# Performance work log

Hardware: AMD Instinct MI355X
Metric: run time of the kernel (lower is better)

## Reference

```python
import jax, jax.numpy as jnp
import numpy as np

B, S, NH, HD = 2, 4096, 16, 64


def setup_inputs() -> dict:
    key = jax.random.key(0)
    kq, kk, kv = jax.random.split(key, 3)
    q = jax.random.normal(kq, (B, S, NH, HD), dtype=jnp.float32)
    k = jax.random.normal(kk, (B, S, NH, HD), dtype=jnp.float32)
    v = jax.random.normal(kv, (B, S, NH, HD), dtype=jnp.float32)
    return {"q": q, "k": k, "v": v}


def reference(q, k, v):
    # SDPA.__call__ with attention_mask=None, segment_ids=None, is_causal=True, dropout=identity
    q_len, nheads, kv_len = q.shape[-3], q.shape[-2], k.shape[-3]
    qs = q / jnp.sqrt(jnp.asarray(q.shape[-1], q.dtype))
    scores = jnp.einsum('...tnh,...snh->...tns', qs, k)  # [B, q, nheads, kv]
    # causal mask: tril over (q, kv), broadcast over heads axis (-2)
    causal = jnp.tril(jnp.ones((q_len, kv_len), dtype=jnp.bool_))[:, None, :]
    neg_inf = jnp.finfo(scores.dtype).min
    scores = jnp.where(causal, scores, neg_inf)
    weights = jax.nn.softmax(scores.astype(jnp.float32), axis=-1).astype(scores.dtype)
    attn = jnp.einsum('...tns,...snh->...tnh', weights, v)
    return attn
```

## Files before the change

kernel.cpp:

```cpp
#include <hip/hip_runtime.h>


constexpr int BATCH  = 2;
constexpr int SEQ    = 4096;
constexpr int NHEADS = 16;
constexpr int HDIM   = 64;
constexpr int ROWSTR = NHEADS * HDIM;
constexpr int BM     = 128;
constexpr int BN     = 64;
constexpr int QTILES = SEQ / BM;
constexpr int BH     = BATCH * NHEADS;

typedef __attribute__((ext_vector_type(8)))  short v8s;
typedef __attribute__((ext_vector_type(16))) float v16f;
typedef __attribute__((ext_vector_type(4)))  unsigned int v4u;
typedef __attribute__((ext_vector_type(2)))  unsigned int v2u;
typedef __attribute__((ext_vector_type(2)))  __bf16 v2bf;

__device__ __forceinline__ unsigned pkbf(float a, float b) {
#if __has_builtin(__builtin_amdgcn_cvt_pk_bf16_f32)
    return __builtin_bit_cast(unsigned, __builtin_amdgcn_cvt_pk_bf16_f32(a, b));
#else
    unsigned ua = __float_as_uint(a); ua += 0x7FFFu + ((ua >> 16) & 1u);
    unsigned ub = __float_as_uint(b); ub += 0x7FFFu + ((ub >> 16) & 1u);
    return (ua >> 16) | (ub & 0xFFFF0000u);
#endif
}

__device__ __forceinline__ int fswz(int r) { return (r & 7) ^ ((r >> 3) & 3); }

__device__ __forceinline__ void async16(const unsigned short* g, unsigned short* l) {
    __builtin_amdgcn_global_load_lds(
        (const __attribute__((address_space(1))) unsigned int*)g,
        (__attribute__((address_space(3))) unsigned int*)l, 16, 0, 0);
}

__global__ __launch_bounds__(256, 4)
void prep(const float* __restrict__ kf, const float* __restrict__ vf,
          unsigned short* __restrict__ kb, unsigned short* __restrict__ vt)
{
    __shared__ unsigned int lds[128 * 33];
    const int tid = threadIdx.x;
    const int blk = (int)blockIdx.x;

    if (blk < 1024) {
        const float4* src = (const float4*)kf + (size_t)blk * 2048;
        unsigned int* dst = (unsigned int*)kb + (size_t)blk * 4096;
        #pragma unroll
        for (int i = 0; i < 8; ++i) {
            const int n = i * 256 + tid;
            float4 f = src[n];
            *(v2u*)(dst + (size_t)n * 2) = (v2u){pkbf(f.x, f.y), pkbf(f.z, f.w)};
        }
        return;
    }

    const int t  = blk - 1024;
    const int b  = t >> 9;
    const int h  = (t >> 5) & 15;
    const int s0 = (t & 31) * 128;

    {
        const float4* vff = (const float4*)vf + (size_t)b * SEQ * 256;
        const int c2 = (tid & 15) * 2;
        #pragma unroll
        for (int i = 0; i < 8; ++i) {
            const int srow = i * 16 + (tid >> 4);
            float4 f = vff[(size_t)(s0 + srow) * 256 + h * 16 + (tid & 15)];
            lds[srow * 33 + c2]     = pkbf(f.x, f.y);
            lds[srow * 33 + c2 + 1] = pkbf(f.z, f.w);
        }
    }
    __syncthreads();
    {
        const int w    = tid >> 6;
        const int lane = tid & 63;
        const int sh   = (lane & 1) * 16;
        const unsigned int* lcol = &lds[w * 32 * 33 + (lane >> 1)];
        unsigned int out[16];
        #pragma unroll
        for (int j = 0; j < 16; ++j) {
            const unsigned a = lcol[(2 * j)     * 33];
            const unsigned c = lcol[(2 * j + 1) * 33];
            out[j] = ((a >> sh) & 0xFFFFu) | (((c >> sh) & 0xFFFFu) << 16);
        }
        unsigned int* dst = (unsigned int*)vt
            + ((size_t)((b * NHEADS + h) * HDIM + lane)) * (SEQ / 2)
            + ((s0 + w * 32) >> 1);
        #pragma unroll
        for (int j = 0; j < 4; ++j)
            *(v4u*)(dst + 4 * j) = (v4u){out[4*j], out[4*j+1], out[4*j+2], out[4*j+3]};
    }
}

__global__ __launch_bounds__(256, 4)
void fa_fwd(const float* __restrict__ qf, const unsigned short* __restrict__ kb,
            const unsigned short* __restrict__ vt, float* __restrict__ og)
{
    __shared__ __align__(16) unsigned short k_s[2][64 * 64];
    __shared__ __align__(16) unsigned short v_s[2][64 * 64];

    const int tid  = threadIdx.x;
    const int wave = tid >> 6;
    const int lane = tid & 63;
    const int hh   = lane >> 5;
    const int l32  = lane & 31;

    const int n  = (int)blockIdx.x;
    const int qtile = QTILES - 1 - (n >> 5);
    const int bh = n & 31;
    const int b = bh >> 4, h = bh & 15;
    const int qbase = qtile * BM;
    const int jmax  = 2 * qtile + 2;

    const int lrow  = lane >> 3;
    const int lcol8 = (lane & 7) ^ lrow ^ wave;
    const int fx = (l32 & 7) ^ ((l32 >> 3) & 3);

    {
        const int krow = tid >> 2;
        const int kc   = (tid & 3) * 16;
        const int sg0  = (2 * (tid & 3))     ^ fswz(krow);
        const int sg1  = (2 * (tid & 3) + 1) ^ fswz(krow);
        const float sc = 0.125f * 1.44269504088896340736f;
        #pragma unroll
        for (int half = 0; half < 2; ++half) {
            const float4* src = (const float4*)(qf +
                ((size_t)((b * SEQ + qbase + half * 64 + krow) * NHEADS + h)) * HDIM + kc);
            float4 f0 = src[0], f1 = src[1], f2 = src[2], f3 = src[3];
            unsigned short* dst = half ? &v_s[0][krow * 64] : &k_s[0][krow * 64];
            *(v4u*)&dst[sg0 * 8] = (v4u){pkbf(f0.x*sc, f0.y*sc), pkbf(f0.z*sc, f0.w*sc),
                                         pkbf(f1.x*sc, f1.y*sc), pkbf(f1.z*sc, f1.w*sc)};
            *(v4u*)&dst[sg1 * 8] = (v4u){pkbf(f2.x*sc, f2.y*sc), pkbf(f2.z*sc, f2.w*sc),
                                         pkbf(f3.x*sc, f3.y*sc), pkbf(f3.z*sc, f3.w*sc)};
        }
    }
    __syncthreads();
    v8s bq[4];
    {
        const int R = wave * 32 + l32;
        const unsigned short* qrow = (R < 64) ? &k_s[0][R * 64] : &v_s[0][(R - 64) * 64];
        #pragma unroll
        for (int c = 0; c < 4; ++c)
            bq[c] = *(const v8s*)&qrow[(((2*c + hh) ^ fswz(R & 63)) * 8)];
    }
    __syncthreads();

    const unsigned short* kgb = kb + (size_t)b * SEQ * ROWSTR + (size_t)h * HDIM;
    const unsigned short* vgb = vt + (size_t)bh * HDIM * SEQ;

    #pragma unroll
    for (int i = 0; i < 2; ++i) {
        const int rbase = i * 32 + wave * 8;
        async16(kgb + (size_t)(rbase + lrow) * ROWSTR + lcol8 * 8, &k_s[0][rbase * 64]);
        async16(vgb + (size_t)(rbase + lrow) * SEQ    + lcol8 * 8, &v_s[0][rbase * 64]);
    }

    const v16f vzero = (v16f)(0.f);
    v16f o_acc[2];
    o_acc[0] = (v16f)(0.f); o_acc[1] = (v16f)(0.f);
    float l_lane = 0.f;
    const int q_abs = qbase + wave * 32 + l32;

#if __has_builtin(__builtin_amdgcn_fdot2_f32_bf16)
    const v2bf ones2 = __builtin_bit_cast(v2bf, 0x3F803F80u);
#endif

    for (int jt = 0; jt < jmax; ++jt) {
        const int buf = jt & 1;
        __syncthreads();

        if (jt + 1 < jmax) {
            const int nb  = (jt + 1) & 1;
            const int kb2 = (jt + 1) * BN;
            #pragma unroll
            for (int i = 0; i < 2; ++i) {
                const int rbase = i * 32 + wave * 8;
                async16(kgb + (size_t)(kb2 + rbase + lrow) * ROWSTR + lcol8 * 8, &k_s[nb][rbase * 64]);
                async16(vgb + (size_t)(rbase + lrow) * SEQ + kb2    + lcol8 * 8, &v_s[nb][rbase * 64]);
            }
        }

        v16f sacc[2];
        __builtin_amdgcn_s_setprio(1);
        #pragma unroll
        for (int mt = 0; mt < 2; ++mt) {
            const int r = mt * 32 + l32;
            {
                v8s ak = *(const v8s*)&k_s[buf][r * 64 + ((hh ^ fx) * 8)];
                sacc[mt] = __builtin_amdgcn_mfma_f32_32x32x16_bf16(ak, bq[0], vzero, 0, 0, 0);
            }
            #pragma unroll
            for (int c = 1; c < 4; ++c) {
                v8s ak = *(const v8s*)&k_s[buf][r * 64 + (((2*c + hh) ^ fx) * 8)];
                sacc[mt] = __builtin_amdgcn_mfma_f32_32x32x16_bf16(ak, bq[c], sacc[mt], 0, 0, 0);
            }
        }
        __builtin_amdgcn_s_setprio(0);

        const bool masked = (jt >= jmax - 2);
        v8s pf4[4];

        auto exppack = [&](v16f& sc, v8s& d0, v8s& d1, int kofs) {
            #pragma unroll
            for (int r = 0; r < 16; ++r) {
                float pv = __builtin_amdgcn_exp2f(sc[r]);
                if (masked) {
                    const int k_abs = kofs + (r & 3) + 8 * (r >> 2) + 4 * hh;
                    pv = (k_abs > q_abs) ? 0.f : pv;
                }
                sc[r] = pv;
#if !__has_builtin(__builtin_amdgcn_fdot2_f32_bf16)
                l_lane += pv;
#endif
            }
            #pragma unroll
            for (int cc = 0; cc < 2; ++cc) {
                const unsigned lo0 = pkbf(sc[8*cc+0], sc[8*cc+1]);
                const unsigned lo1 = pkbf(sc[8*cc+2], sc[8*cc+3]);
                const unsigned hi0 = pkbf(sc[8*cc+4], sc[8*cc+5]);
                const unsigned hi1 = pkbf(sc[8*cc+6], sc[8*cc+7]);
#if __has_builtin(__builtin_amdgcn_fdot2_f32_bf16)
                l_lane = __builtin_amdgcn_fdot2_f32_bf16(__builtin_bit_cast(v2bf, lo0), ones2, l_lane, false);
                l_lane = __builtin_amdgcn_fdot2_f32_bf16(__builtin_bit_cast(v2bf, lo1), ones2, l_lane, false);
                l_lane = __builtin_amdgcn_fdot2_f32_bf16(__builtin_bit_cast(v2bf, hi0), ones2, l_lane, false);
                l_lane = __builtin_amdgcn_fdot2_f32_bf16(__builtin_bit_cast(v2bf, hi1), ones2, l_lane, false);
#endif
#if __has_builtin(__builtin_amdgcn_permlane32_swap)
                auto r0 = __builtin_amdgcn_permlane32_swap(lo0, hi0, false, false);
                auto r1 = __builtin_amdgcn_permlane32_swap(lo1, hi1, false, false);
                (cc ? d1 : d0) = __builtin_bit_cast(v8s, (v4u){r0[0], r1[0], r0[1], r1[1]});
#else
                const unsigned s0 = hh ? lo0 : hi0;
                const unsigned s1 = hh ? lo1 : hi1;
                const unsigned t0 = (unsigned)__shfl_xor((int)s0, 32, 64);
                const unsigned t1 = (unsigned)__shfl_xor((int)s1, 32, 64);
                v4u w;
                w.x = hh ? t0 : lo0;
                w.y = hh ? t1 : lo1;
                w.z = hh ? hi0 : t0;
                w.w = hh ? hi1 : t1;
                (cc ? d1 : d0) = __builtin_bit_cast(v8s, w);
#endif
            }
        };

        exppack(sacc[0], pf4[0], pf4[1], jt * 64);

        __builtin_amdgcn_s_setprio(1);
        #pragma unroll
        for (int nt = 0; nt < 2; ++nt) {
            const int r = nt * 32 + l32;
            #pragma unroll
            for (int c = 0; c < 2; ++c) {
                v8s bv = *(const v8s*)&v_s[buf][r * 64 + (((2*c + hh) ^ fx) * 8)];
                o_acc[nt] = __builtin_amdgcn_mfma_f32_32x32x16_bf16(pf4[c], bv, o_acc[nt], 0, 0, 0);
            }
        }
        __builtin_amdgcn_s_setprio(0);

        exppack(sacc[1], pf4[2], pf4[3], jt * 64 + 32);

        __builtin_amdgcn_s_setprio(1);
        #pragma unroll
        for (int nt = 0; nt < 2; ++nt) {
            const int r = nt * 32 + l32;
            #pragma unroll
            for (int c = 2; c < 4; ++c) {
                v8s bv = *(const v8s*)&v_s[buf][r * 64 + (((2*c + hh) ^ fx) * 8)];
                o_acc[nt] = __builtin_amdgcn_mfma_f32_32x32x16_bf16(pf4[c], bv, o_acc[nt], 0, 0, 0);
            }
        }
        __builtin_amdgcn_s_setprio(0);
    }

    const float lt = l_lane + __shfl_xor(l_lane, 32);

    #pragma unroll
    for (int r = 0; r < 16; ++r) {
        const int q_local = (r & 3) + 8 * (r >> 2) + 4 * hh;
        const float inv_l = 1.0f / __shfl(lt, q_local, 32);
        const int qrow = qbase + wave * 32 + q_local;
        float* dst = og + ((size_t)((b * SEQ + qrow) * NHEADS + h)) * HDIM + l32;
        dst[0]  = o_acc[0][r] * inv_l;
        dst[32] = o_acc[1][r] * inv_l;
    }
}

extern "C" void kernel_launch(void* const* d_in, const int* in_sizes, int n_in,
                              void* d_out, int out_size, void* d_ws, size_t ws_size,
                              hipStream_t stream) {
    const float* q = (const float*)d_in[0];
    const float* k = (const float*)d_in[1];
    const float* v = (const float*)d_in[2];
    float* out = (float*)d_out;

    const size_t TEN = (size_t)BATCH * NHEADS * SEQ * HDIM;
    unsigned short* kbuf = (unsigned short*)d_ws;
    unsigned short* vbuf = kbuf + TEN;

    prep<<<2048, 256, 0, stream>>>(k, v, kbuf, vbuf);
    fa_fwd<<<QTILES * BH, 256, 0, stream>>>(q, kbuf, vbuf, out);
}
```

Measured before the change: 240.9 us.

## Split long causal query tiles across two blocks and combine partial outputs

For the 16 longest causal query tiles, the KV loop is split into two chunks handled by separate blocks. Each chunk writes its unnormalized output and row sums to workspace, and a new combine kernel adds the pairs and normalizes them. The goal is to cut the critical path set by the longest-running blocks in the causally imbalanced grid. The cost is an extra kernel launch plus workspace traffic for the partials. A fallback path that reorders tile scheduling is used when the workspace is too small.

```diff
diff --git a/kernel.cpp b/kernel.cpp
--- a/kernel.cpp
+++ b/kernel.cpp
@@ -10,6 +10,7 @@
 constexpr int BN     = 64;
 constexpr int QTILES = SEQ / BM;
 constexpr int BH     = BATCH * NHEADS;
+constexpr int NSLOT  = 16 * 2 * BH;
 
 typedef __attribute__((ext_vector_type(8)))  short v8s;
 typedef __attribute__((ext_vector_type(16))) float v16f;
@@ -95,7 +96,8 @@
 
 __global__ __launch_bounds__(256, 4)
 void fa_fwd(const float* __restrict__ qf, const unsigned short* __restrict__ kb,
-            const unsigned short* __restrict__ vt, float* __restrict__ og)
+            const unsigned short* __restrict__ vt, float* __restrict__ og,
+            float* __restrict__ Opart, float* __restrict__ lpart, int mode)
 {
     __shared__ __align__(16) unsigned short k_s[2][64 * 64];
     __shared__ __align__(16) unsigned short v_s[2][64 * 64];
@@ -107,11 +109,30 @@
     const int l32  = lane & 31;
 
     const int n  = (int)blockIdx.x;
-    const int qtile = QTILES - 1 - (n >> 5);
     const int bh = n & 31;
+    const int g  = n >> 5;
+    int qtile, j0, j1, slot = -1;
+    if (mode == 1) {
+        if (g < 32) {
+            qtile = 31 - (g >> 1);
+            const int chunk = g & 1;
+            const int ha = qtile + 1;
+            j0 = chunk ? ha : 0;
+            j1 = chunk ? (2 * qtile + 2) : ha;
+            slot = ((qtile - 16) * 2 + chunk) * BH + bh;
+        } else {
+            qtile = 15 - (g - 32);
+            j0 = 0; j1 = 2 * qtile + 2;
+        }
+    } else {
+        const int rr = g >> 3, xx = g & 7;
+        qtile = (rr == 0) ? 31 - xx : (rr == 1) ? 16 + xx : (rr == 2) ? 15 - xx : xx;
+        j0 = 0; j1 = 2 * qtile + 2;
+    }
     const int b = bh >> 4, h = bh & 15;
     const int qbase = qtile * BM;
-    const int jmax  = 2 * qtile + 2;
+    const int jmaxg = 2 * qtile + 2;
+    const int jcnt  = j1 - j0;
 
     const int lrow  = lane >> 3;
     const int lcol8 = (lane & 7) ^ lrow ^ wave;
@@ -152,8 +173,8 @@
     #pragma unroll
     for (int i = 0; i < 2; ++i) {
         const int rbase = i * 32 + wave * 8;
-        async16(kgb + (size_t)(rbase + lrow) * ROWSTR + lcol8 * 8, &k_s[0][rbase * 64]);
-        async16(vgb + (size_t)(rbase + lrow) * SEQ    + lcol8 * 8, &v_s[0][rbase * 64]);
+        async16(kgb + (size_t)(j0 * BN + rbase + lrow) * ROWSTR + lcol8 * 8, &k_s[0][rbase * 64]);
+        async16(vgb + (size_t)(rbase + lrow) * SEQ + j0 * BN    + lcol8 * 8, &v_s[0][rbase * 64]);
     }
 
     const v16f vzero = (v16f)(0.f);
@@ -166,12 +187,13 @@
     const v2bf ones2 = __builtin_bit_cast(v2bf, 0x3F803F80u);
 #endif
 
-    for (int jt = 0; jt < jmax; ++jt) {
-        const int buf = jt & 1;
+    for (int jl = 0; jl < jcnt; ++jl) {
+        const int jt  = j0 + jl;
+        const int buf = jl & 1;
         __syncthreads();
 
-        if (jt + 1 < jmax) {
-            const int nb  = (jt + 1) & 1;
+        if (jl + 1 < jcnt) {
+            const int nb  = (jl + 1) & 1;
             const int kb2 = (jt + 1) * BN;
             #pragma unroll
             for (int i = 0; i < 2; ++i) {
@@ -198,7 +220,7 @@
         }
         __builtin_amdgcn_s_setprio(0);
 
-        const bool masked = (jt >= jmax - 2);
+        const bool masked = (jt >= jmaxg - 2);
         v8s pf4[4];
 
         auto exppack = [&](v16f& sc, v8s& d0, v8s& d1, int kofs) {
@@ -276,14 +298,60 @@
 
     const float lt = l_lane + __shfl_xor(l_lane, 32);
 
+    if (slot >= 0) {
+        if (hh == 0) lpart[slot * BM + wave * 32 + l32] = lt;
+        float* obase = Opart + (size_t)slot * (BM * HDIM);
+        #pragma unroll
+        for (int r = 0; r < 16; ++r) {
+            const int q_local = (r & 3) + 8 * (r >> 2) + 4 * hh;
+            float* dst = obase + (wave * 32 + q_local) * HDIM + l32;
+            dst[0]  = o_acc[0][r];
+            dst[32] = o_acc[1][r];
+        }
+    } else {
+        #pragma unroll
+        for (int r = 0; r < 16; ++r) {
+            const int q_local = (r & 3) + 8 * (r >> 2) + 4 * hh;
+            const float inv_l = 1.0f / __shfl(lt, q_local, 32);
+            const int qrow = qbase + wave * 32 + q_local;
+            float* dst = og + ((size_t)((b * SEQ + qrow) * NHEADS + h)) * HDIM + l32;
+            dst[0]  = o_acc[0][r] * inv_l;
+            dst[32] = o_acc[1][r] * inv_l;
+        }
+    }
+}
+
+__global__ __launch_bounds__(256, 8)
+void combine(const float* __restrict__ Opart, const float* __restrict__ lpart,
+             float* __restrict__ og)
+{
+    __shared__ float linv[BM];
+    const int tid = threadIdx.x;
+    const int blk = (int)blockIdx.x;
+    const int qtile = 16 + (blk >> 5);
+    const int bh = blk & 31;
+    const int b = bh >> 4, h = bh & 15;
+    const int slotA = ((qtile - 16) * 2 + 0) * BH + bh;
+    const int slotB = slotA + BH;
+
+    if (tid < BM)
+        linv[tid] = 1.0f / (lpart[slotA * BM + tid] + lpart[slotB * BM + tid]);
+    __syncthreads();
+
+    const float4* pa = (const float4*)(Opart + (size_t)slotA * (BM * HDIM));
+    const float4* pb = (const float4*)(Opart + (size_t)slotB * (BM * HDIM));
+    const int qbase = qtile * BM;
     #pragma unroll
-    for (int r = 0; r < 16; ++r) {
-        const int q_local = (r & 3) + 8 * (r >> 2) + 4 * hh;
-        const float inv_l = 1.0f / __shfl(lt, q_local, 32);
-        const int qrow = qbase + wave * 32 + q_local;
-        float* dst = og + ((size_t)((b * SEQ + qrow) * NHEADS + h)) * HDIM + l32;
-        dst[0]  = o_acc[0][r] * inv_l;
-        dst[32] = o_acc[1][r] * inv_l;
+    for (int i = 0; i < 8; ++i) {
+        const int e  = i * 256 + tid;
+        const int q  = e >> 4;
+        const int c4 = e & 15;
+        float4 a = pa[e], bb = pb[e];
+        const float s = linv[q];
+        float4 o; o.x = (a.x + bb.x) * s; o.y = (a.y + bb.y) * s;
+                  o.z = (a.z + bb.z) * s; o.w = (a.w + bb.w) * s;
+        float4* dst = (float4*)(og + ((size_t)((b * SEQ + qbase + q) * NHEADS + h)) * HDIM) + c4;
+        *dst = o;
     }
 }
 
@@ -298,7 +366,18 @@
     const size_t TEN = (size_t)BATCH * NHEADS * SEQ * HDIM;
     unsigned short* kbuf = (unsigned short*)d_ws;
     unsigned short* vbuf = kbuf + TEN;
+    float* Opart = (float*)(vbuf + TEN);
+    float* lpart = Opart + (size_t)NSLOT * (BM * HDIM);
+
+    const size_t need = TEN * 2 * sizeof(unsigned short)
+                      + ((size_t)NSLOT * (BM * HDIM) + (size_t)NSLOT * BM) * sizeof(float);
+    const int mode = (ws_size >= need) ? 1 : 0;
 
     prep<<<2048, 256, 0, stream>>>(k, v, kbuf, vbuf);
-    fa_fwd<<<QTILES * BH, 256, 0, stream>>>(q, kbuf, vbuf, out);
-}
+    if (mode == 1) {
+        fa_fwd<<<48 * BH, 256, 0, stream>>>(q, kbuf, vbuf, out, Opart, lpart, 1);
+        combine<<<16 * BH, 256, 0, stream>>>(Opart, lpart, out);
+    } else {
+        fa_fwd<<<QTILES * BH, 256, 0, stream>>>(q, kbuf, vbuf, out, Opart, lpart, 0);
+    }
+}
```

After: 253.9 us. 5.4% more time.
